# Kernel tuning notes

Hardware: AMD Instinct MI355X
Metric: run time of the kernel (lower is better)

Reference implementation:

```python
import jax, jax.numpy as jnp
import numpy as np

N_NODES = 50000
N_EDGES = 800000
D_IN = 128
D_HID = 128
D_OUT = 40
NUM_LAYERS = 2


def _sage_conv(x, src, dst, W_l, b_l, W_r, num_nodes):
    # PyG SAGEConv (aggr='mean'): out = lin_l(mean_{j in N(i)} x_j) + lin_r(x_i)
    msg = x[src]                                              # [E, d] gather
    agg = jax.ops.segment_sum(msg, dst, num_segments=num_nodes)  # [N, d] scatter-add
    deg = jax.ops.segment_sum(jnp.ones_like(dst, dtype=x.dtype), dst,
                              num_segments=num_nodes)
    agg = agg / jnp.clip(deg, 1.0)[:, None]                   # mean (deg>=1 clamp)
    return agg @ W_l.T + b_l + x @ W_r.T


def setup_inputs() -> dict:
    key = jax.random.key(0)
    ks = jax.random.split(key, 10)
    x = jax.random.normal(ks[0], (N_NODES, D_IN), dtype=jnp.float32)
    edge_index = jax.random.randint(ks[1], (2, N_EDGES), 0, N_NODES, dtype=jnp.int64)
    s = 1.0 / np.sqrt(D_IN)
    W1_l = jax.random.uniform(ks[2], (D_HID, D_IN), jnp.float32, -s, s)
    b1_l = jax.random.uniform(ks[3], (D_HID,), jnp.float32, -s, s)
    W1_r = jax.random.uniform(ks[4], (D_HID, D_IN), jnp.float32, -s, s)
    sh = 1.0 / np.sqrt(D_HID)
    W2_l = jax.random.uniform(ks[5], (D_HID, D_HID), jnp.float32, -sh, sh)
    b2_l = jax.random.uniform(ks[6], (D_HID,), jnp.float32, -sh, sh)
    W2_r = jax.random.uniform(ks[7], (D_HID, D_HID), jnp.float32, -sh, sh)
    sc = 1.0 / np.sqrt(D_HID * NUM_LAYERS)
    W_lin = jax.random.uniform(ks[8], (D_OUT, D_HID * NUM_LAYERS), jnp.float32, -sc, sc)
    b_lin = jax.random.uniform(ks[9], (D_OUT,), jnp.float32, -sc, sc)
    return {"x": x, "edge_index": edge_index,
            "W1_l": W1_l, "b1_l": b1_l, "W1_r": W1_r,
            "W2_l": W2_l, "b2_l": b2_l, "W2_r": W2_r,
            "W_lin": W_lin, "b_lin": b_lin}


def reference(x, edge_index, W1_l, b1_l, W1_r, W2_l, b2_l, W2_r, W_lin, b_lin):
    src, dst = edge_index[0], edge_index[1]
    n = x.shape[0]
    h1 = jax.nn.relu(_sage_conv(x, src, dst, W1_l, b1_l, W1_r, n))   # dropout: eval mode -> identity
    h2 = jax.nn.relu(_sage_conv(h1, src, dst, W2_l, b2_l, W2_r, n))
    h_cat = jnp.concatenate([h1, h2], axis=1)                        # [N, 2*hid]
    logits = h_cat @ W_lin.T + b_lin                                 # [N, out]
    return jax.nn.log_softmax(logits, axis=1)
```

## Files before the change

### kernel.cpp

```cpp
#include <hip/hip_runtime.h>
#include <math.h>

#define N_NODES 50000
#define N_EDGES 800000
#define D 128
#define NBLK 196

typedef __attribute__((ext_vector_type(8))) short bf16x8;
typedef __attribute__((ext_vector_type(4))) float f32x4;
typedef __attribute__((ext_vector_type(4))) unsigned int u32x4;

static __device__ __forceinline__ unsigned short f2bf(float f) {
    unsigned int u = __float_as_uint(f);
    u = (u + 0x7fffu + ((u >> 16) & 1u)) >> 16;
    return (unsigned short)u;
}
static __device__ __forceinline__ float bf2f(unsigned short h) {
    return __uint_as_float(((unsigned int)h) << 16);
}

__global__ void prep_deg_kernel(const int* __restrict__ dst, int* __restrict__ deg,
                                int* __restrict__ rank,
                                const float* __restrict__ x,
                                const float* __restrict__ W1l, const float* __restrict__ W1r,
                                const float* __restrict__ W2l, const float* __restrict__ W2r,
                                const float* __restrict__ Wlin,
                                unsigned short* __restrict__ xhi, unsigned short* __restrict__ xlo,
                                unsigned short* __restrict__ W1hi, unsigned short* __restrict__ W1lo,
                                unsigned short* __restrict__ W2hi, unsigned short* __restrict__ W2lo,
                                unsigned short* __restrict__ WLhi, unsigned short* __restrict__ WLlo) {
    int b = blockIdx.x, tid = threadIdx.x;
    if (b < 3125) {
        int e = b * 256 + tid;
        rank[e] = atomicAdd(&deg[dst[e]], 1);
    } else if (b < 9375) {
        int i = ((b - 3125) * 256 + tid) * 4;
        float4 v = *(const float4*)(x + i);
        ushort4 h, l;
        h.x = f2bf(v.x); l.x = f2bf(v.x - bf2f(h.x));
        h.y = f2bf(v.y); l.y = f2bf(v.y - bf2f(h.y));
        h.z = f2bf(v.z); l.z = f2bf(v.z - bf2f(h.z));
        h.w = f2bf(v.w); l.w = f2bf(v.w - bf2f(h.w));
        *(ushort4*)(xhi + i) = h;
        *(ushort4*)(xlo + i) = l;
    } else if (b < 9503) {
        int isW2 = (b >= 9439);
        const float* A = isW2 ? W2l : W1l;
        const float* B = isW2 ? W2r : W1r;
        unsigned short* hi = isW2 ? W2hi : W1hi;
        unsigned short* lo = isW2 ? W2lo : W1lo;
        int f = (b - (isW2 ? 9439 : 9375)) * 2 + (tid >> 7);
        int t = tid & 127;
        float va = A[f * 128 + t], vb = B[f * 128 + t];
        unsigned short ha = f2bf(va), hb = f2bf(vb);
        hi[f * 256 + t]       = ha;
        hi[f * 256 + 128 + t] = hb;
        lo[f * 256 + t]       = f2bf(va - bf2f(ha));
        lo[f * 256 + 128 + t] = f2bf(vb - bf2f(hb));
    } else {
        int f = b - 9503;
        float v = (f < 40) ? Wlin[f * 256 + tid] : 0.f;
        unsigned short h = f2bf(v);
        WLhi[f * 256 + tid] = h;
        WLlo[f * 256 + tid] = f2bf(v - bf2f(h));
    }
}

__global__ void scan_partial(const int* __restrict__ deg, int* __restrict__ bsum) {
    __shared__ int wt[4];
    int tid = threadIdx.x, lane = tid & 63, wv = tid >> 6;
    int idx = blockIdx.x * 256 + tid;
    int v = (idx < N_NODES) ? deg[idx] : 0;
    int s = v;
    #pragma unroll
    for (int o = 1; o < 64; o <<= 1) s += __shfl_xor(s, o, 64);
    if (lane == 0) wt[wv] = s;
    __syncthreads();
    if (tid == 0) bsum[blockIdx.x] = wt[0] + wt[1] + wt[2] + wt[3];
}

__global__ void scan_write(const int* __restrict__ deg, const int* __restrict__ bsum,
                           int* __restrict__ rowptr) {
    __shared__ int wt[4], wt2[4];
    int tid = threadIdx.x, lane = tid & 63, wv = tid >> 6;
    int v0 = (tid < blockIdx.x) ? bsum[tid] : 0;
    int s0 = v0;
    #pragma unroll
    for (int o = 1; o < 64; o <<= 1) s0 += __shfl_xor(s0, o, 64);
    if (lane == 0) wt2[wv] = s0;
    int idx = blockIdx.x * 256 + tid;
    int v = (idx < N_NODES) ? deg[idx] : 0;
    int s = v;
    #pragma unroll
    for (int o = 1; o < 64; o <<= 1) { int t = __shfl_up(s, o, 64); if (lane >= o) s += t; }
    if (lane == 63) wt[wv] = s;
    __syncthreads();
    int boff = wt2[0] + wt2[1] + wt2[2] + wt2[3];
    #pragma unroll
    for (int w = 0; w < 4; w++) boff += (w < wv) ? wt[w] : 0;
    int excl = boff + s - v;
    if (idx < N_NODES) rowptr[idx] = excl;
    if (idx == 0) rowptr[N_NODES] = N_EDGES;
}

__global__ void bucket_kernel(const int* __restrict__ src, const int* __restrict__ dst,
                              const int* __restrict__ rowptr, const int* __restrict__ rank,
                              int* __restrict__ srcs_sorted) {
    int e = blockIdx.x * blockDim.x + threadIdx.x;
    if (e < N_EDGES) {
        srcs_sorted[rowptr[dst[e]] + rank[e]] = src[e];
    }
}

template<bool FINAL>
__global__ __launch_bounds__(512, 4) void fused_layer(
    const int* __restrict__ srcs, const int* __restrict__ rowptr,
    const unsigned short* __restrict__ Shi,
    const unsigned short* __restrict__ A2hi, const unsigned short* __restrict__ A2lo,
    const unsigned short* __restrict__ Whi, const unsigned short* __restrict__ Wlo,
    const float* __restrict__ bias,
    unsigned short* __restrict__ Ohi, unsigned short* __restrict__ Olo,
    const unsigned short* __restrict__ WLhi, const unsigned short* __restrict__ WLlo,
    const float* __restrict__ blin, float* __restrict__ out)
{
    __shared__ unsigned int Ah[64 * 68];
    __shared__ unsigned int Al[64 * 68];
    __shared__ unsigned short Wl[8192];
    __shared__ float stats[256];

    const int tid = threadIdx.x;
    const int wv = tid >> 6, lane = tid & 63;
    const int nb0 = blockIdx.x * 64;

    const int nclamp = min(nb0 + lane, N_NODES - 1);
    const int rp0 = rowptr[nclamp];
    const int rp1 = rowptr[nclamp + 1];

    const char* xb = (const char*)Shi;
    const int g = lane >> 4;
    const int q = lane & 15;
    const int qb = q << 4;
    #pragma unroll 1
    for (int it = 0; it < 4; it++) {
        int nlA = it * 16 + wv, nlB = nlA + 8;
        int begA = __shfl(rp0, nlA, 64), endA = __shfl(rp1, nlA, 64);
        int begB = __shfl(rp0, nlB, 64), endB = __shfl(rp1, nlB, 64);
        int degA = endA - begA, degB = endB - begB;
        float ax[4] = {0,0,0,0}, ay[4] = {0,0,0,0};
        float bx[4] = {0,0,0,0}, by[4] = {0,0,0,0};
        int nsA = (degA + 63) >> 6, nsB = (degB + 63) >> 6;
        int nsmax = max(nsA, nsB);
        #pragma unroll 1
        for (int st = 0; st < nsmax; st++) {
            int svA = 0, svB = 0;
            int nbA = 0, nbB = 0;
            if (st < nsA) {
                int sb = begA + (st << 6);
                nbA = min(64, endA - sb);
                svA = srcs[min(sb + lane, endA - 1)];
            }
            if (st < nsB) {
                int sb = begB + (st << 6);
                nbB = min(64, endB - sb);
                svB = srcs[min(sb + lane, endB - 1)];
            }
            int itA = (nbA + 3) >> 2, itB = (nbB + 3) >> 2;
            int itmax = max(itA, itB);
            #pragma unroll 4
            for (int b = 0; b < itmax; b++) {
                int ei = (b << 2) + g;
                if (b < itA) {
                    unsigned srcv = (unsigned)__shfl(svA, ei, 64);
                    u32x4 v = *(const u32x4*)(xb + ((srcv << 8) + qb));
                    v.x = (ei < nbA) ? v.x : 0u;
                    v.y = (ei < nbA) ? v.y : 0u;
                    v.z = (ei < nbA) ? v.z : 0u;
                    v.w = (ei < nbA) ? v.w : 0u;
                    ax[0] += __uint_as_float(v.x << 16); ay[0] += __uint_as_float(v.x & 0xffff0000u);
                    ax[1] += __uint_as_float(v.y << 16); ay[1] += __uint_as_float(v.y & 0xffff0000u);
                    ax[2] += __uint_as_float(v.z << 16); ay[2] += __uint_as_float(v.z & 0xffff0000u);
                    ax[3] += __uint_as_float(v.w << 16); ay[3] += __uint_as_float(v.w & 0xffff0000u);
                }
                if (b < itB) {
                    unsigned srcv = (unsigned)__shfl(svB, ei, 64);
                    u32x4 v = *(const u32x4*)(xb + ((srcv << 8) + qb));
                    v.x = (ei < nbB) ? v.x : 0u;
                    v.y = (ei < nbB) ? v.y : 0u;
                    v.z = (ei < nbB) ? v.z : 0u;
                    v.w = (ei < nbB) ? v.w : 0u;
                    bx[0] += __uint_as_float(v.x << 16); by[0] += __uint_as_float(v.x & 0xffff0000u);
                    bx[1] += __uint_as_float(v.y << 16); by[1] += __uint_as_float(v.y & 0xffff0000u);
                    bx[2] += __uint_as_float(v.z << 16); by[2] += __uint_as_float(v.z & 0xffff0000u);
                    bx[3] += __uint_as_float(v.w << 16); by[3] += __uint_as_float(v.w & 0xffff0000u);
                }
            }
        }
        #pragma unroll
        for (int d = 0; d < 4; d++) {
            ax[d] += __shfl_xor(ax[d], 16, 64); ax[d] += __shfl_xor(ax[d], 32, 64);
            ay[d] += __shfl_xor(ay[d], 16, 64); ay[d] += __shfl_xor(ay[d], 32, 64);
            bx[d] += __shfl_xor(bx[d], 16, 64); bx[d] += __shfl_xor(bx[d], 32, 64);
            by[d] += __shfl_xor(by[d], 16, 64); by[d] += __shfl_xor(by[d], 32, 64);
        }
        if (g == 0) {
            float invA = 1.0f / fmaxf((float)degA, 1.0f);
            float invB = 1.0f / fmaxf((float)degB, 1.0f);
            u32x4 ha, la, hb, lb;
            #pragma unroll
            for (int d = 0; d < 4; d++) {
                float sx = ax[d] * invA, sy = ay[d] * invA;
                unsigned short h0 = f2bf(sx), h1 = f2bf(sy);
                unsigned short l0 = f2bf(sx - bf2f(h0)), l1 = f2bf(sy - bf2f(h1));
                ha[d] = (unsigned)h0 | ((unsigned)h1 << 16);
                la[d] = (unsigned)l0 | ((unsigned)l1 << 16);
                float tx = bx[d] * invB, ty = by[d] * invB;
                unsigned short h2 = f2bf(tx), h3 = f2bf(ty);
                unsigned short l2 = f2bf(tx - bf2f(h2)), l3 = f2bf(ty - bf2f(h3));
                hb[d] = (unsigned)h2 | ((unsigned)h3 << 16);
                lb[d] = (unsigned)l2 | ((unsigned)l3 << 16);
            }
            *(u32x4*)&Ah[nlA * 68 + q * 4] = ha;
            *(u32x4*)&Al[nlA * 68 + q * 4] = la;
            *(u32x4*)&Ah[nlB * 68 + q * 4] = hb;
            *(u32x4*)&Al[nlB * 68 + q * 4] = lb;
        }
    }
    __syncthreads();

    const int m = lane & 15, quad = lane >> 4;
    const int gg = wv & 3, tp = wv >> 2;
    const int node_base = nb0 + gg * 16;
    const int nodec = min(node_base + m, N_NODES - 1);

    bf16x8 a1h[4], a1l[4], a2h[4], a2l[4];
    {
        const unsigned short* r2h = A2hi + (size_t)nodec * D + quad * 8;
        const unsigned short* r2l = A2lo + (size_t)nodec * D + quad * 8;
        #pragma unroll
        for (int ks = 0; ks < 4; ks++) {
            a2h[ks] = *(const bf16x8*)(r2h + ks * 32);
            a2l[ks] = *(const bf16x8*)(r2l + ks * 32);
        }
        #pragma unroll
        for (int ks = 0; ks < 4; ks++) {
            int ad = ((gg * 16 + m) * 68 + quad * 4 + ks * 16) * 2;
            a1h[ks] = *(const bf16x8*)((const unsigned short*)Ah + ad);
            a1l[ks] = *(const bf16x8*)((const unsigned short*)Al + ad);
        }
    }

    #pragma unroll 1
    for (int fq = 0; fq < 4; fq++) {
        const int f0 = fq * 32;
        if (fq) __syncthreads();
        #pragma unroll
        for (int itS = 0; itS < 2; itS++) {
            int c = tid + itS * 512;
            int nt = c >> 9, w2 = c & 511;
            int ks = w2 >> 6, lidx = w2 & 63;
            int mm = lidx >> 2, qq = lidx & 3;
            const unsigned short* gp = Whi + (size_t)(f0 + nt * 16 + mm) * 256 + ks * 32 + qq * 8;
            *(bf16x8*)&Wl[(size_t)c * 8] = *(const bf16x8*)gp;
        }
        __syncthreads();

        int f = f0 + tp * 16 + m;
        const unsigned short* wlorow = Wlo + (size_t)f * 256 + quad * 8;
        f32x4 acc0 = {0.f, 0.f, 0.f, 0.f};
        f32x4 acc1 = {0.f, 0.f, 0.f, 0.f};
        f32x4 acc2 = {0.f, 0.f, 0.f, 0.f};
        #pragma unroll
        for (int ks = 0; ks < 8; ks++) {
            bf16x8 bh = *(const bf16x8*)&Wl[(size_t)(((tp * 8 + ks) << 6) + (m * 4 + quad)) * 8];
            bf16x8 bl = *(const bf16x8*)(wlorow + ks * 32);
            bf16x8 ah = (ks < 4) ? a1h[ks] : a2h[ks - 4];
            bf16x8 al = (ks < 4) ? a1l[ks] : a2l[ks - 4];
            acc0 = __builtin_amdgcn_mfma_f32_16x16x32_bf16(ah, bh, acc0, 0, 0, 0);
            acc1 = __builtin_amdgcn_mfma_f32_16x16x32_bf16(ah, bl, acc1, 0, 0, 0);
            acc2 = __builtin_amdgcn_mfma_f32_16x16x32_bf16(al, bh, acc2, 0, 0, 0);
        }
        float bv = bias[f];
        #pragma unroll
        for (int r = 0; r < 4; r++) {
            int lrow = gg * 16 + quad * 4 + r;
            int nrow = nb0 + lrow;
            float v = fmaxf((acc0[r] + (acc1[r] + acc2[r])) + bv, 0.f);
            unsigned short h = f2bf(v);
            unsigned short l = f2bf(v - bf2f(h));
            if (FINAL) {
                ((unsigned short*)Ah)[lrow * 136 + f] = h;
                ((unsigned short*)Al)[lrow * 136 + f] = l;
            } else if (nrow < N_NODES) {
                Ohi[(size_t)nrow * D + f] = h;
                Olo[(size_t)nrow * D + f] = l;
            }
        }
    }

    if (!FINAL) return;

    __syncthreads();
    bf16x8 a3h[4], a3l[4];
    #pragma unroll
    for (int ks = 0; ks < 4; ks++) {
        int ad = (gg * 16 + m) * 136 + ks * 32 + quad * 8;
        a3h[ks] = *(const bf16x8*)((const unsigned short*)Ah + ad);
        a3l[ks] = *(const bf16x8*)((const unsigned short*)Al + ad);
    }
    const int ntiles = (tp == 0) ? 2 : 1;
    float res[2][4];
    #pragma unroll
    for (int t = 0; t < 2; t++) {
        if (t >= ntiles) break;
        int nt = (tp == 0) ? t : 2;
        int f = nt * 16 + m;
        const unsigned short* whirow = WLhi + (size_t)f * 256 + quad * 8;
        const unsigned short* wlorow = WLlo + (size_t)f * 256 + quad * 8;
        f32x4 acc0 = {0.f, 0.f, 0.f, 0.f};
        f32x4 acc1 = {0.f, 0.f, 0.f, 0.f};
        f32x4 acc2 = {0.f, 0.f, 0.f, 0.f};
        #pragma unroll
        for (int ks = 0; ks < 8; ks++) {
            bf16x8 bh = *(const bf16x8*)(whirow + ks * 32);
            bf16x8 bl = *(const bf16x8*)(wlorow + ks * 32);
            bf16x8 ah = (ks < 4) ? a2h[ks] : a3h[ks - 4];
            bf16x8 al = (ks < 4) ? a2l[ks] : a3l[ks - 4];
            acc0 = __builtin_amdgcn_mfma_f32_16x16x32_bf16(ah, bh, acc0, 0, 0, 0);
            acc1 = __builtin_amdgcn_mfma_f32_16x16x32_bf16(ah, bl, acc1, 0, 0, 0);
            acc2 = __builtin_amdgcn_mfma_f32_16x16x32_bf16(al, bh, acc2, 0, 0, 0);
        }
        float bv = (f < 40) ? blin[f] : 0.f;
        #pragma unroll
        for (int r = 0; r < 4; r++) res[t][r] = (acc0[r] + (acc1[r] + acc2[r])) + bv;
    }
    #pragma unroll
    for (int r = 0; r < 4; r++) {
        float pm = -INFINITY;
        #pragma unroll
        for (int t = 0; t < 2; t++) {
            if (t >= ntiles) break;
            int f = ((tp == 0) ? t : 2) * 16 + m;
            if (f < 40) pm = fmaxf(pm, res[t][r]);
        }
        #pragma unroll
        for (int o = 8; o > 0; o >>= 1) pm = fmaxf(pm, __shfl_xor(pm, o, 64));
        if (m == 0) stats[tp * 64 + gg * 16 + quad * 4 + r] = pm;
    }
    __syncthreads();
    float gm[4];
    #pragma unroll
    for (int r = 0; r < 4; r++) {
        int row = gg * 16 + quad * 4 + r;
        gm[r] = fmaxf(stats[row], stats[64 + row]);
        float ps = 0.f;
        #pragma unroll
        for (int t = 0; t < 2; t++) {
            if (t >= ntiles) break;
            int f = ((tp == 0) ? t : 2) * 16 + m;
            if (f < 40) ps += expf(res[t][r] - gm[r]);
        }
        #pragma unroll
        for (int o = 8; o > 0; o >>= 1) ps += __shfl_xor(ps, o, 64);
        if (m == 0) stats[128 + tp * 64 + row] = ps;
    }
    __syncthreads();
    #pragma unroll
    for (int r = 0; r < 4; r++) {
        int row = gg * 16 + quad * 4 + r;
        int nrow = nb0 + row;
        if (nrow >= N_NODES) continue;
        float lse = gm[r] + logf(stats[128 + row] + stats[192 + row]);
        #pragma unroll
        for (int t = 0; t < 2; t++) {
            if (t >= ntiles) break;
            int f = ((tp == 0) ? t : 2) * 16 + m;
            if (f < 40) out[(size_t)nrow * 40 + f] = res[t][r] - lse;
        }
    }
}

extern "C" void kernel_launch(void* const* d_in, const int* in_sizes, int n_in,
                              void* d_out, int out_size, void* d_ws, size_t ws_size,
                              hipStream_t stream) {
    const float* x     = (const float*)d_in[0];
    const int*   ei    = (const int*)d_in[1];
    const int*   src   = ei;
    const int*   dst   = ei + N_EDGES;
    const float* W1_l  = (const float*)d_in[2];
    const float* b1_l  = (const float*)d_in[3];
    const float* W1_r  = (const float*)d_in[4];
    const float* W2_l  = (const float*)d_in[5];
    const float* b2_l  = (const float*)d_in[6];
    const float* W2_r  = (const float*)d_in[7];
    const float* W_lin = (const float*)d_in[8];
    const float* b_lin = (const float*)d_in[9];
    float* out = (float*)d_out;

    const size_t nd = (size_t)N_NODES * D;
    unsigned short* xhi  = (unsigned short*)d_ws;
    unsigned short* xlo  = xhi + nd;
    unsigned short* h1hi = xlo + nd;
    unsigned short* h1lo = h1hi + nd;
    unsigned short* W1hi = h1lo + nd;
    unsigned short* W1lo = W1hi + 128 * 256;
    unsigned short* W2hi = W1lo + 128 * 256;
    unsigned short* W2lo = W2hi + 128 * 256;
    unsigned short* WLhi = W2lo + 128 * 256;
    unsigned short* WLlo = WLhi + 48 * 256;
    int* deg    = (int*)(WLlo + 48 * 256);
    int* rowptr = deg + N_NODES;
    int* rank   = rowptr + N_NODES + 1;
    int* srcs_sorted = rank + N_EDGES;
    int* bsum   = srcs_sorted + N_EDGES;

    hipMemsetAsync(deg, 0, N_NODES * sizeof(int), stream);
    prep_deg_kernel<<<9551, 256, 0, stream>>>(dst, deg, rank, x, W1_l, W1_r, W2_l, W2_r, W_lin,
                                              xhi, xlo, W1hi, W1lo, W2hi, W2lo, WLhi, WLlo);

    scan_partial<<<NBLK, 256, 0, stream>>>(deg, bsum);
    scan_write<<<NBLK, 256, 0, stream>>>(deg, bsum, rowptr);
    bucket_kernel<<<(N_EDGES + 255) / 256, 256, 0, stream>>>(src, dst, rowptr, rank, srcs_sorted);

    const int lblk = (N_NODES + 63) / 64;

    fused_layer<false><<<lblk, 512, 0, stream>>>(srcs_sorted, rowptr, xhi, xhi, xlo,
                                                 W1hi, W1lo, b1_l, h1hi, h1lo,
                                                 nullptr, nullptr, nullptr, nullptr);
    fused_layer<true><<<lblk, 512, 0, stream>>>(srcs_sorted, rowptr, h1hi, h1hi, h1lo,
                                                W2hi, W2lo, b2_l, nullptr, nullptr,
                                                WLhi, WLlo, b_lin, out);
}
```

Baseline: 339.7 us.

## Split fused gather+GEMM layer into separate persistent gather and GEMM kernels

Separates the neighbour-mean gather from the GEMM. The gather becomes a grid-stride kernel with 256-thread blocks, where each wave handles a pair of adjacent nodes and writes hi/lo bf16 aggregates to a global workspace. The GEMM kernel then reads those aggregates from global memory instead of shared memory. The aim is higher occupancy and better load balance for the latency-bound gather, paid for by an extra global write and read of the aggregated features plus two more launches.

Result: faster. 329.3 us (-3.0%).

```diff
diff --git a/kernel.cpp b/kernel.cpp
--- a/kernel.cpp
+++ b/kernel.cpp
@@ -5,6 +5,7 @@
 #define N_EDGES 800000
 #define D 128
 #define NBLK 196
+#define GATHER_BLOCKS 2048
 
 typedef __attribute__((ext_vector_type(8))) short bf16x8;
 typedef __attribute__((ext_vector_type(4))) float f32x4;
@@ -112,48 +113,33 @@
     }
 }
 
-template<bool FINAL>
-__global__ __launch_bounds__(512, 4) void fused_layer(
+__global__ __launch_bounds__(256, 8) void gather_mean(
     const int* __restrict__ srcs, const int* __restrict__ rowptr,
     const unsigned short* __restrict__ Shi,
-    const unsigned short* __restrict__ A2hi, const unsigned short* __restrict__ A2lo,
-    const unsigned short* __restrict__ Whi, const unsigned short* __restrict__ Wlo,
-    const float* __restrict__ bias,
-    unsigned short* __restrict__ Ohi, unsigned short* __restrict__ Olo,
-    const unsigned short* __restrict__ WLhi, const unsigned short* __restrict__ WLlo,
-    const float* __restrict__ blin, float* __restrict__ out)
+    unsigned short* __restrict__ Aghi, unsigned short* __restrict__ Aglo)
 {
-    __shared__ unsigned int Ah[64 * 68];
-    __shared__ unsigned int Al[64 * 68];
-    __shared__ unsigned short Wl[8192];
-    __shared__ float stats[256];
-
     const int tid = threadIdx.x;
     const int wv = tid >> 6, lane = tid & 63;
-    const int nb0 = blockIdx.x * 64;
-
-    const int nclamp = min(nb0 + lane, N_NODES - 1);
-    const int rp0 = rowptr[nclamp];
-    const int rp1 = rowptr[nclamp + 1];
-
+    const int g = lane >> 4, q = lane & 15;
+    const int qb = q << 4;
     const char* xb = (const char*)Shi;
-    const int g = lane >> 4;
-    const int q = lane & 15;
-    const int qb = q << 4;
+    const int wid = blockIdx.x * 4 + wv;
+    const int NW = GATHER_BLOCKS * 4;
     #pragma unroll 1
-    for (int it = 0; it < 4; it++) {
-        int nlA = it * 16 + wv, nlB = nlA + 8;
-        int begA = __shfl(rp0, nlA, 64), endA = __shfl(rp1, nlA, 64);
-        int begB = __shfl(rp0, nlB, 64), endB = __shfl(rp1, nlB, 64);
-        int degA = endA - begA, degB = endB - begB;
+    for (int p = wid; p < N_NODES / 2; p += NW) {
+        const int nA = 2 * p, nB = 2 * p + 1;
+        const int begA = rowptr[nA];
+        const int endA = rowptr[nA + 1];
+        const int endB = rowptr[nB + 1];
+        const int begB = endA;
+        const int degA = endA - begA, degB = endB - begB;
         float ax[4] = {0,0,0,0}, ay[4] = {0,0,0,0};
         float bx[4] = {0,0,0,0}, by[4] = {0,0,0,0};
         int nsA = (degA + 63) >> 6, nsB = (degB + 63) >> 6;
         int nsmax = max(nsA, nsB);
         #pragma unroll 1
         for (int st = 0; st < nsmax; st++) {
-            int svA = 0, svB = 0;
-            int nbA = 0, nbB = 0;
+            int svA = 0, svB = 0, nbA = 0, nbB = 0;
             if (st < nsA) {
                 int sb = begA + (st << 6);
                 nbA = min(64, endA - sb);
@@ -166,12 +152,12 @@
             }
             int itA = (nbA + 3) >> 2, itB = (nbB + 3) >> 2;
             int itmax = max(itA, itB);
-            #pragma unroll 4
+            #pragma unroll 2
             for (int b = 0; b < itmax; b++) {
                 int ei = (b << 2) + g;
                 if (b < itA) {
-                    unsigned srcv = (unsigned)__shfl(svA, ei, 64);
-                    u32x4 v = *(const u32x4*)(xb + ((srcv << 8) + qb));
+                    unsigned sv = (unsigned)__shfl(svA, ei, 64);
+                    u32x4 v = *(const u32x4*)(xb + ((sv << 8) + qb));
                     v.x = (ei < nbA) ? v.x : 0u;
                     v.y = (ei < nbA) ? v.y : 0u;
                     v.z = (ei < nbA) ? v.z : 0u;
@@ -182,8 +168,8 @@
                     ax[3] += __uint_as_float(v.w << 16); ay[3] += __uint_as_float(v.w & 0xffff0000u);
                 }
                 if (b < itB) {
-                    unsigned srcv = (unsigned)__shfl(svB, ei, 64);
-                    u32x4 v = *(const u32x4*)(xb + ((srcv << 8) + qb));
+                    unsigned sv = (unsigned)__shfl(svB, ei, 64);
+                    u32x4 v = *(const u32x4*)(xb + ((sv << 8) + qb));
                     v.x = (ei < nbB) ? v.x : 0u;
                     v.y = (ei < nbB) ? v.y : 0u;
                     v.z = (ei < nbB) ? v.z : 0u;
@@ -219,33 +205,48 @@
                 hb[d] = (unsigned)h2 | ((unsigned)h3 << 16);
                 lb[d] = (unsigned)l2 | ((unsigned)l3 << 16);
             }
-            *(u32x4*)&Ah[nlA * 68 + q * 4] = ha;
-            *(u32x4*)&Al[nlA * 68 + q * 4] = la;
-            *(u32x4*)&Ah[nlB * 68 + q * 4] = hb;
-            *(u32x4*)&Al[nlB * 68 + q * 4] = lb;
-        }
-    }
-    __syncthreads();
-
+            *(u32x4*)(Aghi + (size_t)nA * D + q * 8) = ha;
+            *(u32x4*)(Aglo + (size_t)nA * D + q * 8) = la;
+            *(u32x4*)(Aghi + (size_t)nB * D + q * 8) = hb;
+            *(u32x4*)(Aglo + (size_t)nB * D + q * 8) = lb;
+        }
+    }
+}
+
+template<bool FINAL>
+__global__ __launch_bounds__(512, 4) void gemm_layer(
+    const unsigned short* __restrict__ Aghi, const unsigned short* __restrict__ Aglo,
+    const unsigned short* __restrict__ A2hi, const unsigned short* __restrict__ A2lo,
+    const unsigned short* __restrict__ Whi, const unsigned short* __restrict__ Wlo,
+    const float* __restrict__ bias,
+    unsigned short* __restrict__ Ohi, unsigned short* __restrict__ Olo,
+    const unsigned short* __restrict__ WLhi, const unsigned short* __restrict__ WLlo,
+    const float* __restrict__ blin, float* __restrict__ out)
+{
+    __shared__ unsigned short Wl[8192];
+    __shared__ unsigned int Ah[FINAL ? 64 * 68 : 1];
+    __shared__ unsigned int Al[FINAL ? 64 * 68 : 1];
+    __shared__ float stats[256];
+
+    const int tid = threadIdx.x;
+    const int wv = tid >> 6, lane = tid & 63;
+    const int nb0 = blockIdx.x * 64;
     const int m = lane & 15, quad = lane >> 4;
     const int gg = wv & 3, tp = wv >> 2;
-    const int node_base = nb0 + gg * 16;
-    const int nodec = min(node_base + m, N_NODES - 1);
+    const int nodec = min(nb0 + gg * 16 + m, N_NODES - 1);
 
     bf16x8 a1h[4], a1l[4], a2h[4], a2l[4];
     {
+        const unsigned short* r1h = Aghi + (size_t)nodec * D + quad * 8;
+        const unsigned short* r1l = Aglo + (size_t)nodec * D + quad * 8;
         const unsigned short* r2h = A2hi + (size_t)nodec * D + quad * 8;
         const unsigned short* r2l = A2lo + (size_t)nodec * D + quad * 8;
         #pragma unroll
         for (int ks = 0; ks < 4; ks++) {
+            a1h[ks] = *(const bf16x8*)(r1h + ks * 32);
+            a1l[ks] = *(const bf16x8*)(r1l + ks * 32);
             a2h[ks] = *(const bf16x8*)(r2h + ks * 32);
             a2l[ks] = *(const bf16x8*)(r2l + ks * 32);
-        }
-        #pragma unroll
-        for (int ks = 0; ks < 4; ks++) {
-            int ad = ((gg * 16 + m) * 68 + quad * 4 + ks * 16) * 2;
-            a1h[ks] = *(const bf16x8*)((const unsigned short*)Ah + ad);
-            a1l[ks] = *(const bf16x8*)((const unsigned short*)Al + ad);
         }
     }
 
@@ -412,6 +413,8 @@
     int* rank   = rowptr + N_NODES + 1;
     int* srcs_sorted = rank + N_EDGES;
     int* bsum   = srcs_sorted + N_EDGES;
+    unsigned short* aghi = (unsigned short*)(bsum + NBLK);
+    unsigned short* aglo = aghi + nd;
 
     hipMemsetAsync(deg, 0, N_NODES * sizeof(int), stream);
     prep_deg_kernel<<<9551, 256, 0, stream>>>(dst, deg, rank, x, W1_l, W1_r, W2_l, W2_r, W_lin,
@@ -423,10 +426,12 @@
 
     const int lblk = (N_NODES + 63) / 64;
 
-    fused_layer<false><<<lblk, 512, 0, stream>>>(srcs_sorted, rowptr, xhi, xhi, xlo,
-                                                 W1hi, W1lo, b1_l, h1hi, h1lo,
-                                                 nullptr, nullptr, nullptr, nullptr);
-    fused_layer<true><<<lblk, 512, 0, stream>>>(srcs_sorted, rowptr, h1hi, h1hi, h1lo,
-                                                W2hi, W2lo, b2_l, nullptr, nullptr,
-                                                WLhi, WLlo, b_lin, out);
-}
+    gather_mean<<<GATHER_BLOCKS, 256, 0, stream>>>(srcs_sorted, rowptr, xhi, aghi, aglo);
+    gemm_layer<false><<<lblk, 512, 0, stream>>>(aghi, aglo, xhi, xlo,
+                                                W1hi, W1lo, b1_l, h1hi, h1lo,
+                                                nullptr, nullptr, nullptr, nullptr);
+    gather_mean<<<GATHER_BLOCKS, 256, 0, stream>>>(srcs_sorted, rowptr, h1hi, aghi, aglo);
+    gemm_layer<true><<<lblk, 512, 0, stream>>>(aghi, aglo, h1hi, h1lo,
+                                               W2hi, W2lo, b2_l, nullptr, nullptr,
+                                               WLhi, WLlo, b_lin, out);
+}
```
